# Kernel tuning notes

Hardware: AMD Instinct MI355X
Metric: run time of the kernel (lower is better)

The kernel has to match this reference:

```python
import jax, jax.numpy as jnp
import numpy as np

N_NODE = 2000
N_EDGE = 100000
N_REL2 = 102  # num_relation * 2
D_IN = 64
N_TRI = 500000


def _triangles(src, dst, N):
    """Faithful numpy port of triangle_list: for each edge (a,c) intersect
    out-neighbors of a with in-neighbors of c via sorted edge lists + searchsorted.
    Returns (edge_ab, edge_bc, edge_ac) edge-index triples."""
    E = len(src)
    src = src.astype(np.int64); dst = dst.astype(np.int64)
    in_order = np.argsort(src * N + dst, kind='stable')   # edges sorted by (a,b)
    out_order = np.argsort(dst * N + src, kind='stable')  # edges sorted by (c,b)
    deg_in = np.bincount(src, minlength=N)
    deg_out = np.bincount(dst, minlength=N)
    neighbor_out = dst[in_order]
    neighbor_in = src[out_order]
    cum_in = np.concatenate([[0], np.cumsum(deg_in)])
    cum_out = np.concatenate([[0], np.cumsum(deg_out)])
    # candidate b's: out-neighbors of a, replicated per edge (a,c)
    cnt_a = deg_in[src]
    ce = np.repeat(np.arange(E), cnt_a)
    offs = np.arange(cnt_a.sum()) - np.repeat(np.cumsum(cnt_a) - cnt_a, cnt_a)
    pos = np.repeat(cum_in[src], cnt_a) + offs
    b = neighbor_out[pos]
    ab_cand = in_order[pos]
    # boundary: in-neighbors of c, replicated per edge (globally sorted via N*segment offset)
    cnt_c = deg_out[dst]
    se = np.repeat(np.arange(E), cnt_c)
    offs2 = np.arange(cnt_c.sum()) - np.repeat(np.cumsum(cnt_c) - cnt_c, cnt_c)
    pos2 = np.repeat(cum_out[dst], cnt_c) + offs2
    boundary = neighbor_in[pos2] + N * se
    bc_order = out_order[pos2]
    key = b + N * ce
    left = np.searchsorted(boundary, key, side='left')
    right = np.searchsorted(boundary, key, side='right')
    count = right - left
    rep = np.repeat(np.arange(len(count)), count)
    within = np.arange(count.sum()) - np.repeat(np.cumsum(count) - count, count)
    return ab_cand[rep], bc_order[left[rep] + within], ce[rep]


def setup_inputs() -> dict:
    rng = np.random.default_rng(0)
    src = rng.integers(0, N_NODE, N_EDGE)
    dst = rng.integers(0, N_NODE, N_EDGE)
    edge_type = rng.integers(0, N_REL2, N_EDGE)
    ab, bc, ac = _triangles(src, dst, N_NODE)
    if len(ab) == 0:  # pathological fallback
        ab = rng.integers(0, N_EDGE, N_TRI)
        bc = rng.integers(0, N_EDGE, N_TRI)
        ac = rng.integers(0, N_EDGE, N_TRI)
    sel = rng.integers(0, len(ab), N_TRI)  # fixed-size (re)sample of triangles
    s = 0.1
    return {
        'edge_type': jnp.asarray(edge_type, jnp.int64) if jax.config.jax_enable_x64 else jnp.asarray(edge_type, jnp.int32),
        'edge_ab': jnp.asarray(ab[sel], jnp.int32),
        'edge_bc': jnp.asarray(bc[sel], jnp.int32),
        'edge_ac': jnp.asarray(ac[sel], jnp.int32),
        'fact_emb': jnp.asarray(rng.standard_normal((N_REL2, D_IN)) * s, jnp.float32),
        'W1': jnp.asarray(rng.standard_normal((D_IN, D_IN)) * s, jnp.float32),
        'b1': jnp.zeros((D_IN,), jnp.float32),
        'W2': jnp.asarray(rng.standard_normal((D_IN, D_IN)) * s, jnp.float32),
        'b2': jnp.zeros((D_IN,), jnp.float32),
        'mlp_W1': jnp.asarray(rng.standard_normal((2 * D_IN, 2 * D_IN)) * s, jnp.float32),
        'mlp_b1': jnp.zeros((2 * D_IN,), jnp.float32),
        'mlp_W2': jnp.asarray(rng.standard_normal((2 * D_IN, 1)) * s, jnp.float32),
        'mlp_b2': jnp.zeros((1,), jnp.float32),
    }


def reference(edge_type, edge_ab, edge_bc, edge_ac, fact_emb,
              W1, b1, W2, b2, mlp_W1, mlp_b1, mlp_W2, mlp_b2):
    E = edge_type.shape[0]
    x0 = fact_emb[edge_type]                      # [E, d] initial edge (fact) features
    x = x0
    for W, b in ((W1, b1), (W2, b2)):
        msg = x[edge_ab] * x[edge_bc]             # [T, d] distmult triangle messages
        agg = jax.ops.segment_sum(msg, edge_ac, num_segments=E)  # scatter-add onto ac edge
        x = jax.nn.relu(agg @ W + b)              # per-layer linear + activation
    feat = jnp.concatenate([x, x0], axis=-1)      # [E, 2d] (hidden + input, concat_hidden=False)
    h = jax.nn.relu(feat @ mlp_W1 + mlp_b1)
    return (h @ mlp_W2 + mlp_b2)[:, 0]            # [E] per-edge score
```

## Files before the change

kernel.cpp:

```cpp
#include <hip/hip_runtime.h>

#define D 64
#define FPAD 65

__device__ __forceinline__ float relu_f(float v) { return v > 0.f ? v : 0.f; }

__global__ __launch_bounds__(256) void k_prep(int* __restrict__ cnt, int En,
        const float* __restrict__ fe, const float* __restrict__ W1,
        float* __restrict__ P, int nrel,
        const float* __restrict__ mW1, const float* __restrict__ mb1,
        float* __restrict__ Q, int nZ, int nP) {
    __shared__ float Wl[64 * 64];
    __shared__ float fT[64 * FPAD];
    const int tid = threadIdx.x;
    int b = blockIdx.x;

    if (b < nZ) {
        int i = (b * 256 + tid) * 4;
        if (i + 3 < En) {
            *reinterpret_cast<int4*>(cnt + i) = make_int4(0, 0, 0, 0);
        } else {
            for (int k = i; k < En; ++k) cnt[k] = 0;
        }
        return;
    }
    b -= nZ;
    if (b < nP) {
        const int npair = nrel * nrel;
        const int p0 = b * 64;

        for (int i = tid; i < 1024; i += 256)
            reinterpret_cast<float4*>(Wl)[i] = reinterpret_cast<const float4*>(W1)[i];

        for (int i = tid; i < 1024; i += 256) {
            int r = i >> 4, q = i & 15;
            int p = p0 + r;
            float4 v = make_float4(0.f, 0.f, 0.f, 0.f);
            if (p < npair) {
                int pa = p / nrel, pb = p - pa * nrel;
                float4 va = reinterpret_cast<const float4*>(fe + (size_t)pa * D)[q];
                float4 vb = reinterpret_cast<const float4*>(fe + (size_t)pb * D)[q];
                v = make_float4(va.x * vb.x, va.y * vb.y, va.z * vb.z, va.w * vb.w);
            }
            fT[(q * 4 + 0) * FPAD + r] = v.x;
            fT[(q * 4 + 1) * FPAD + r] = v.y;
            fT[(q * 4 + 2) * FPAD + r] = v.z;
            fT[(q * 4 + 3) * FPAD + r] = v.w;
        }
        __syncthreads();

        const int j0 = (tid & 15) * 4;
        const int r0 = (tid >> 4) * 4;
        float acc[4][4];
        #pragma unroll
        for (int i = 0; i < 4; ++i)
            #pragma unroll
            for (int j = 0; j < 4; ++j) acc[i][j] = 0.f;

        #pragma unroll 8
        for (int k = 0; k < 64; ++k) {
            float4 f = *reinterpret_cast<const float4*>(&fT[k * FPAD + r0]);
            float4 w = *reinterpret_cast<const float4*>(&Wl[k * 64 + j0]);
            float fa[4] = {f.x, f.y, f.z, f.w};
            float wa[4] = {w.x, w.y, w.z, w.w};
            #pragma unroll
            for (int i = 0; i < 4; ++i)
                #pragma unroll
                for (int j = 0; j < 4; ++j) acc[i][j] += fa[i] * wa[j];
        }

        #pragma unroll
        for (int i = 0; i < 4; ++i) {
            int p = p0 + r0 + i;
            if (p < npair) {
                float4 o = make_float4(acc[i][0], acc[i][1], acc[i][2], acc[i][3]);
                *reinterpret_cast<float4*>(P + (size_t)p * D + j0) = o;
            }
        }
        return;
    }
    b -= nP;
    int t = b * 2 + (tid >> 7);
    int j = tid & 127;
    float* fl = &fT[(tid >> 7) * 64];
    if (t < nrel && j < 64) fl[j] = fe[(size_t)t * D + j];
    __syncthreads();
    if (t < nrel) {
        float s = mb1[j];
        #pragma unroll 16
        for (int k = 0; k < 64; ++k)
            s += fl[k] * mW1[(size_t)(64 + k) * 128 + j];
        Q[(size_t)t * 128 + j] = s;
    }
}


__global__ void k_hist(const int* __restrict__ ac, int* __restrict__ cnt, int T) {
    int t = blockIdx.x * blockDim.x + threadIdx.x;
    if (t < T) atomicAdd(&cnt[ac[t]], 1);
}

__global__ __launch_bounds__(256) void k_scanA(const int* __restrict__ cnt,
        int* __restrict__ localExcl, int* __restrict__ blockSums, int E) {
    __shared__ int ls[256];
    const int tid = threadIdx.x;
    int base = blockIdx.x * 1024 + tid * 4;
    int a0 = 0, a1 = 0, a2 = 0, a3 = 0;
    if (base + 3 < E) {
        int4 v = *reinterpret_cast<const int4*>(cnt + base);
        a0 = v.x; a1 = v.y; a2 = v.z; a3 = v.w;
    } else {
        if (base + 0 < E) a0 = cnt[base + 0];
        if (base + 1 < E) a1 = cnt[base + 1];
        if (base + 2 < E) a2 = cnt[base + 2];
        if (base + 3 < E) a3 = cnt[base + 3];
    }
    int tsum = a0 + a1 + a2 + a3;
    ls[tid] = tsum;
    __syncthreads();
    for (int off = 1; off < 256; off <<= 1) {
        int v = (tid >= off) ? ls[tid - off] : 0;
        __syncthreads();
        ls[tid] += v;
        __syncthreads();
    }
    int excl = ls[tid] - tsum;
    if (tid == 255) blockSums[blockIdx.x] = ls[255];
    if (base + 3 < E) {
        int4 o = make_int4(excl, excl + a0, excl + a0 + a1, excl + a0 + a1 + a2);
        *reinterpret_cast<int4*>(localExcl + base) = o;
    } else {
        int run = excl;
        if (base + 0 < E) { localExcl[base + 0] = run; run += a0; }
        if (base + 1 < E) { localExcl[base + 1] = run; run += a1; }
        if (base + 2 < E) { localExcl[base + 2] = run; run += a2; }
        if (base + 3 < E) { localExcl[base + 3] = run; }
    }
}

__global__ __launch_bounds__(256) void k_scanC(const int* __restrict__ localExcl,
        const int* __restrict__ blockSums, const int* __restrict__ cnt,
        int2* __restrict__ seg, int* __restrict__ cursor, int E, int nblk) {
    __shared__ int ls[256];
    const int tid = threadIdx.x;
    int v = (tid < nblk) ? blockSums[tid] : 0;
    ls[tid] = v;
    __syncthreads();
    for (int off = 1; off < 256; off <<= 1) {
        int w = (tid >= off) ? ls[tid - off] : 0;
        __syncthreads();
        ls[tid] += w;
        __syncthreads();
    }
    int excl = ls[tid] - v;
    __syncthreads();
    ls[tid] = excl;
    __syncthreads();
    int i = blockIdx.x * blockDim.x + tid;
    if (i < E) {
        int s = localExcl[i] + ls[i >> 10];
        seg[i] = make_int2(s, cnt[i]);
        cursor[i] = s;
    }
}

__global__ void k_permute(const int* __restrict__ ab, const int* __restrict__ bc,
                          const int* __restrict__ ac, const int* __restrict__ et,
                          int* __restrict__ cursor, int2* __restrict__ tri,
                          int* __restrict__ pid, int T, int nrel) {
    int t = blockIdx.x * blockDim.x + threadIdx.x;
    if (t >= T) return;
    int a = ab[t], b = bc[t];
    int pos = atomicAdd(&cursor[ac[t]], 1);
    tri[pos] = make_int2(a, b);
    pid[pos] = et[a] * nrel + et[b];
}

__global__ __launch_bounds__(256) void k_msg1b(const int2* __restrict__ seg,
        const int* __restrict__ pid, const float* __restrict__ P,
        const float* __restrict__ b1, float* __restrict__ xb, int E, int nquad) {
    const int tid = threadIdx.x;
    const int lane = tid & 63;
    const int sub = lane & 15;
    const int grp = lane >> 4;
    const float4* __restrict__ P4 = reinterpret_cast<const float4*>(P);
    const float4 bb = reinterpret_cast<const float4*>(b1)[sub];

    for (int quad = (blockIdx.x * blockDim.x + tid) >> 6; quad * 4 < E; quad += nquad) {
        const int e = quad * 4 + grp;
        int2 sc = make_int2(0, 0);
        if (e < E) sc = seg[e];
        const int s = sc.x, c = sc.y;
        float4 acc = make_float4(0.f, 0.f, 0.f, 0.f);
        int i = 0;
        for (; i + 3 < c; i += 4) {
            int q0 = pid[s + i + 0];
            int q1 = pid[s + i + 1];
            int q2 = pid[s + i + 2];
            int q3 = pid[s + i + 3];
            float4 v0 = P4[(size_t)q0 * 16 + sub];
            float4 v1 = P4[(size_t)q1 * 16 + sub];
            float4 v2 = P4[(size_t)q2 * 16 + sub];
            float4 v3 = P4[(size_t)q3 * 16 + sub];
            acc.x += v0.x + v1.x + v2.x + v3.x;
            acc.y += v0.y + v1.y + v2.y + v3.y;
            acc.z += v0.z + v1.z + v2.z + v3.z;
            acc.w += v0.w + v1.w + v2.w + v3.w;
        }
        for (; i < c; ++i) {
            float4 v = P4[(size_t)pid[s + i] * 16 + sub];
            acc.x += v.x; acc.y += v.y; acc.z += v.z; acc.w += v.w;
        }
        if (e < E) {
            float4 o;
            o.x = relu_f(acc.x + bb.x);
            o.y = relu_f(acc.y + bb.y);
            o.z = relu_f(acc.z + bb.z);
            o.w = relu_f(acc.w + bb.w);
            reinterpret_cast<float4*>(xb + (size_t)e * D)[sub] = o;
        }
    }
}

__global__ __launch_bounds__(256) void k_msg4(const int2* __restrict__ seg,
        const int2* __restrict__ tri, const float* __restrict__ xin,
        float* __restrict__ agg, int E, int nquad) {
    const int tid = threadIdx.x;
    const int lane = tid & 63;
    const int sub = lane & 15;
    const int grp = lane >> 4;
    const float4* __restrict__ x4 = reinterpret_cast<const float4*>(xin);

    for (int quad = (blockIdx.x * blockDim.x + tid) >> 6; quad * 4 < E; quad += nquad) {
        const int e = quad * 4 + grp;
        int2 sc = make_int2(0, 0);
        if (e < E) sc = seg[e];
        const int s = sc.x, c = sc.y;
        float4 acc = make_float4(0.f, 0.f, 0.f, 0.f);
        int i = 0;
        for (; i + 3 < c; i += 4) {
            int2 p0 = tri[s + i + 0];
            int2 p1 = tri[s + i + 1];
            int2 p2 = tri[s + i + 2];
            int2 p3 = tri[s + i + 3];
            float4 va0 = x4[(size_t)p0.x * 16 + sub];
            float4 vb0 = x4[(size_t)p0.y * 16 + sub];
            float4 va1 = x4[(size_t)p1.x * 16 + sub];
            float4 vb1 = x4[(size_t)p1.y * 16 + sub];
            float4 va2 = x4[(size_t)p2.x * 16 + sub];
            float4 vb2 = x4[(size_t)p2.y * 16 + sub];
            float4 va3 = x4[(size_t)p3.x * 16 + sub];
            float4 vb3 = x4[(size_t)p3.y * 16 + sub];
            acc.x += va0.x * vb0.x; acc.y += va0.y * vb0.y;
            acc.z += va0.z * vb0.z; acc.w += va0.w * vb0.w;
            acc.x += va1.x * vb1.x; acc.y += va1.y * vb1.y;
            acc.z += va1.z * vb1.z; acc.w += va1.w * vb1.w;
            acc.x += va2.x * vb2.x; acc.y += va2.y * vb2.y;
            acc.z += va2.z * vb2.z; acc.w += va2.w * vb2.w;
            acc.x += va3.x * vb3.x; acc.y += va3.y * vb3.y;
            acc.z += va3.z * vb3.z; acc.w += va3.w * vb3.w;
        }
        for (; i < c; ++i) {
            int2 p = tri[s + i];
            float4 va = x4[(size_t)p.x * 16 + sub];
            float4 vb = x4[(size_t)p.y * 16 + sub];
            acc.x += va.x * vb.x;
            acc.y += va.y * vb.y;
            acc.z += va.z * vb.z;
            acc.w += va.w * vb.w;
        }
        if (e < E)
            reinterpret_cast<float4*>(agg + (size_t)e * D)[sub] = acc;
    }
}

__global__ __launch_bounds__(256) void k_linmlp(const float* __restrict__ agg,
        const int* __restrict__ et, const float* __restrict__ Q,
        const float* __restrict__ W2, const float* __restrict__ b2,
        const float* __restrict__ mW1, const float* __restrict__ mW2,
        const float* __restrict__ mb2, float* __restrict__ out, int E) {
    __shared__ float Wl[64 * 64];
    __shared__ float fT[64 * FPAD];
    const int tid = threadIdx.x;
    const int row0 = blockIdx.x * 64;
    const int j0 = (tid & 15) * 4;
    const int r0 = (tid >> 4) * 4;

    for (int i = tid; i < 1024; i += 256)
        reinterpret_cast<float4*>(Wl)[i] = reinterpret_cast<const float4*>(W2)[i];
    for (int i = tid; i < 1024; i += 256) {
        int r = i >> 4, q = i & 15;
        float4 v = make_float4(0.f, 0.f, 0.f, 0.f);
        if (row0 + r < E)
            v = reinterpret_cast<const float4*>(agg + (size_t)(row0 + r) * D)[q];
        fT[(q * 4 + 0) * FPAD + r] = v.x;
        fT[(q * 4 + 1) * FPAD + r] = v.y;
        fT[(q * 4 + 2) * FPAD + r] = v.z;
        fT[(q * 4 + 3) * FPAD + r] = v.w;
    }
    __syncthreads();

    float acc[4][4];
    #pragma unroll
    for (int i = 0; i < 4; ++i)
        #pragma unroll
        for (int j = 0; j < 4; ++j) acc[i][j] = 0.f;

    #pragma unroll 8
    for (int k = 0; k < 64; ++k) {
        float4 f = *reinterpret_cast<const float4*>(&fT[k * FPAD + r0]);
        float4 w = *reinterpret_cast<const float4*>(&Wl[k * 64 + j0]);
        float fa[4] = {f.x, f.y, f.z, f.w};
        float wa[4] = {w.x, w.y, w.z, w.w};
        #pragma unroll
        for (int i = 0; i < 4; ++i)
            #pragma unroll
            for (int j = 0; j < 4; ++j) acc[i][j] += fa[i] * wa[j];
    }

    {
        float4 bv = *reinterpret_cast<const float4*>(&b2[j0]);
        float ba[4] = {bv.x, bv.y, bv.z, bv.w};
        #pragma unroll
        for (int i = 0; i < 4; ++i)
            #pragma unroll
            for (int j = 0; j < 4; ++j) acc[i][j] = relu_f(acc[i][j] + ba[j]);
    }

    __syncthreads();

    #pragma unroll
    for (int i = 0; i < 4; ++i)
        #pragma unroll
        for (int j = 0; j < 4; ++j)
            fT[(j0 + j) * FPAD + (r0 + i)] = acc[i][j];
    for (int i = tid; i < 1024; i += 256) {
        int k = i >> 4, q = i & 15;
        reinterpret_cast<float4*>(Wl)[i] =
            *reinterpret_cast<const float4*>(mW1 + (size_t)k * 128 + q * 4);
    }
    __syncthreads();

    int etc_[4];
    #pragma unroll
    for (int i = 0; i < 4; ++i) {
        int row = row0 + r0 + i;
        etc_[i] = (row < E) ? et[row] : 0;
    }

    float p[4] = {0.f, 0.f, 0.f, 0.f};

    {
        float acc2[4][4];
        #pragma unroll
        for (int i = 0; i < 4; ++i)
            #pragma unroll
            for (int j = 0; j < 4; ++j) acc2[i][j] = 0.f;
        #pragma unroll 8
        for (int k = 0; k < 64; ++k) {
            float4 f = *reinterpret_cast<const float4*>(&fT[k * FPAD + r0]);
            float4 w = *reinterpret_cast<const float4*>(&Wl[k * 64 + j0]);
            float fa[4] = {f.x, f.y, f.z, f.w};
            float wa[4] = {w.x, w.y, w.z, w.w};
            #pragma unroll
            for (int i = 0; i < 4; ++i)
                #pragma unroll
                for (int j = 0; j < 4; ++j) acc2[i][j] += fa[i] * wa[j];
        }
        float4 w2v = *reinterpret_cast<const float4*>(&mW2[j0]);
        #pragma unroll
        for (int i = 0; i < 4; ++i) {
            float4 qv = *reinterpret_cast<const float4*>(&Q[(size_t)etc_[i] * 128 + j0]);
            p[i] += relu_f(acc2[i][0] + qv.x) * w2v.x;
            p[i] += relu_f(acc2[i][1] + qv.y) * w2v.y;
            p[i] += relu_f(acc2[i][2] + qv.z) * w2v.z;
            p[i] += relu_f(acc2[i][3] + qv.w) * w2v.w;
        }
    }
    __syncthreads();
    for (int i = tid; i < 1024; i += 256) {
        int k = i >> 4, q = i & 15;
        reinterpret_cast<float4*>(Wl)[i] =
            *reinterpret_cast<const float4*>(mW1 + (size_t)k * 128 + 64 + q * 4);
    }
    __syncthreads();
    {
        float acc2[4][4];
        #pragma unroll
        for (int i = 0; i < 4; ++i)
            #pragma unroll
            for (int j = 0; j < 4; ++j) acc2[i][j] = 0.f;
        #pragma unroll 8
        for (int k = 0; k < 64; ++k) {
            float4 f = *reinterpret_cast<const float4*>(&fT[k * FPAD + r0]);
            float4 w = *reinterpret_cast<const float4*>(&Wl[k * 64 + j0]);
            float fa[4] = {f.x, f.y, f.z, f.w};
            float wa[4] = {w.x, w.y, w.z, w.w};
            #pragma unroll
            for (int i = 0; i < 4; ++i)
                #pragma unroll
                for (int j = 0; j < 4; ++j) acc2[i][j] += fa[i] * wa[j];
        }
        float4 w2v = *reinterpret_cast<const float4*>(&mW2[64 + j0]);
        #pragma unroll
        for (int i = 0; i < 4; ++i) {
            float4 qv = *reinterpret_cast<const float4*>(&Q[(size_t)etc_[i] * 128 + 64 + j0]);
            p[i] += relu_f(acc2[i][0] + qv.x) * w2v.x;
            p[i] += relu_f(acc2[i][1] + qv.y) * w2v.y;
            p[i] += relu_f(acc2[i][2] + qv.z) * w2v.z;
            p[i] += relu_f(acc2[i][3] + qv.w) * w2v.w;
        }
    }

    const float bias2 = mb2[0];
    #pragma unroll
    for (int i = 0; i < 4; ++i) {
        float s = p[i];
        s += __shfl_xor(s, 1, 64);
        s += __shfl_xor(s, 2, 64);
        s += __shfl_xor(s, 4, 64);
        s += __shfl_xor(s, 8, 64);
        if ((tid & 15) == 0) {
            int row = row0 + r0 + i;
            if (row < E) out[row] = s + bias2;
        }
    }
}

extern "C" void kernel_launch(void* const* d_in, const int* in_sizes, int n_in,
                              void* d_out, int out_size, void* d_ws, size_t ws_size,
                              hipStream_t stream) {
    const int*   edge_type = (const int*)d_in[0];
    const int*   ab        = (const int*)d_in[1];
    const int*   bc        = (const int*)d_in[2];
    const int*   ac        = (const int*)d_in[3];
    const float* fe        = (const float*)d_in[4];
    const float* W1        = (const float*)d_in[5];
    const float* b1        = (const float*)d_in[6];
    const float* W2        = (const float*)d_in[7];
    const float* b2        = (const float*)d_in[8];
    const float* mW1       = (const float*)d_in[9];
    const float* mb1       = (const float*)d_in[10];
    const float* mW2       = (const float*)d_in[11];
    const float* mb2       = (const float*)d_in[12];

    const int E = in_sizes[0];
    const int T = in_sizes[1];
    const int nrel = in_sizes[4] / D;
    const int npair = nrel * nrel;
    float* out = (float*)d_out;

    char* p = (char*)d_ws;
    float* xb   = (float*)p;   p += (size_t)E * D * sizeof(float);
    float* agg  = (float*)p;   p += (size_t)E * D * sizeof(float);
    float* P    = (float*)p;   p += (size_t)npair * D * sizeof(float);
    float* Q    = (float*)p;   p += (size_t)nrel * 128 * sizeof(float);
    int* cnt    = (int*)p;     p += (size_t)E * sizeof(int);
    int* lexcl  = (int*)p;     p += (size_t)E * sizeof(int);
    int* cursor = (int*)p;     p += (size_t)E * sizeof(int);
    int* bsums  = (int*)p;     p += 256 * sizeof(int);
    int2* seg   = (int2*)p;    p += (size_t)E * sizeof(int2);
    int2* tri   = (int2*)p;    p += (size_t)T * sizeof(int2);
    int* pid    = (int*)p;     p += (size_t)T * sizeof(int);

    const int nblkA = (E + 1023) / 1024;
    const int nZ = (E + 1023) / 1024;
    const int nP = (npair + 63) / 64;
    const int nQb = (nrel + 1) / 2;

    k_prep<<<nZ + nP + nQb, 256, 0, stream>>>(cnt, E, fe, W1, P, nrel, mW1, mb1, Q, nZ, nP);
    k_hist<<<(T + 255) / 256, 256, 0, stream>>>(ac, cnt, T);
    k_scanA<<<nblkA, 256, 0, stream>>>(cnt, lexcl, bsums, E);
    k_scanC<<<(E + 255) / 256, 256, 0, stream>>>(lexcl, bsums, cnt, seg, cursor, E, nblkA);
    k_permute<<<(T + 255) / 256, 256, 0, stream>>>(ab, bc, ac, edge_type, cursor, tri, pid, T, nrel);

    const int MSG_BLOCKS = 2048;
    const int nquad = MSG_BLOCKS * 256 / 64;
    k_msg1b<<<MSG_BLOCKS, 256, 0, stream>>>(seg, pid, P, b1, xb, E, nquad);
    k_msg4<<<MSG_BLOCKS, 256, 0, stream>>>(seg, tri, xb, agg, E, nquad);
    k_linmlp<<<(E + 63) / 64, 256, 0, stream>>>(agg, edge_type, Q, W2, b2, mW1, mW2, mb2, out, E);
}
```

Measured before the change: 164.4 us.

## Sort edges by triangle count per block for balanced wavefronts; retile MLP GEMM

k_scanC now also does a per-1024-edge-block counting sort of edges by triangle count (capped at 64), writing an order array. Both message kernels walk edges through that order, so the four edges sharing a wavefront have similar loop trip counts and less divergence. Separately, the MLP stage in k_linmlp is retiled to compute all 128 hidden columns in one pass over two K-halves with 8x4 register tiles, replacing two 64-column passes. The cost is an extra indirection load per edge, scattered output writes, and shared-memory atomics in the scan.

```diff
diff --git a/kernel.cpp b/kernel.cpp
--- a/kernel.cpp
+++ b/kernel.cpp
@@ -140,8 +140,10 @@
 
 __global__ __launch_bounds__(256) void k_scanC(const int* __restrict__ localExcl,
         const int* __restrict__ blockSums, const int* __restrict__ cnt,
-        int2* __restrict__ seg, int* __restrict__ cursor, int E, int nblk) {
+        int2* __restrict__ seg, int* __restrict__ cursor, int* __restrict__ order,
+        int E, int nblk) {
     __shared__ int ls[256];
+    __shared__ int bh[65];
     const int tid = threadIdx.x;
     int v = (tid < nblk) ? blockSums[tid] : 0;
     ls[tid] = v;
@@ -155,12 +157,48 @@
     int excl = ls[tid] - v;
     __syncthreads();
     ls[tid] = excl;
-    __syncthreads();
-    int i = blockIdx.x * blockDim.x + tid;
-    if (i < E) {
-        int s = localExcl[i] + ls[i >> 10];
-        seg[i] = make_int2(s, cnt[i]);
-        cursor[i] = s;
+    if (tid < 65) bh[tid] = 0;
+    __syncthreads();
+    const int myoff = ls[blockIdx.x];
+
+    const int base = blockIdx.x * 1024;
+    const int idx0 = base + tid * 4;
+    int c0 = 0, c1 = 0, c2 = 0, c3 = 0;
+    if (idx0 + 3 < E) {
+        int4 cv = *reinterpret_cast<const int4*>(cnt + idx0);
+        c0 = cv.x; c1 = cv.y; c2 = cv.z; c3 = cv.w;
+    } else {
+        if (idx0 + 0 < E) c0 = cnt[idx0 + 0];
+        if (idx0 + 1 < E) c1 = cnt[idx0 + 1];
+        if (idx0 + 2 < E) c2 = cnt[idx0 + 2];
+        if (idx0 + 3 < E) c3 = cnt[idx0 + 3];
+    }
+    int ca[4] = {c0, c1, c2, c3};
+    #pragma unroll
+    for (int k = 0; k < 4; ++k) {
+        int i = idx0 + k;
+        if (i < E) {
+            int s = localExcl[i] + myoff;
+            seg[i] = make_int2(s, ca[k]);
+            cursor[i] = s;
+            int bk = ca[k] < 64 ? ca[k] : 64;
+            atomicAdd(&bh[bk], 1);
+        }
+    }
+    __syncthreads();
+    if (tid == 0) {
+        int run = 0;
+        for (int k = 0; k < 65; ++k) { int t = bh[k]; bh[k] = run; run += t; }
+    }
+    __syncthreads();
+    #pragma unroll
+    for (int k = 0; k < 4; ++k) {
+        int i = idx0 + k;
+        if (i < E) {
+            int bk = ca[k] < 64 ? ca[k] : 64;
+            int pos = atomicAdd(&bh[bk], 1);
+            order[base + pos] = i;
+        }
     }
 }
 
@@ -177,8 +215,9 @@
 }
 
 __global__ __launch_bounds__(256) void k_msg1b(const int2* __restrict__ seg,
-        const int* __restrict__ pid, const float* __restrict__ P,
-        const float* __restrict__ b1, float* __restrict__ xb, int E, int nquad) {
+        const int* __restrict__ order, const int* __restrict__ pid,
+        const float* __restrict__ P, const float* __restrict__ b1,
+        float* __restrict__ xb, int E, int nquad) {
     const int tid = threadIdx.x;
     const int lane = tid & 63;
     const int sub = lane & 15;
@@ -187,9 +226,10 @@
     const float4 bb = reinterpret_cast<const float4*>(b1)[sub];
 
     for (int quad = (blockIdx.x * blockDim.x + tid) >> 6; quad * 4 < E; quad += nquad) {
-        const int e = quad * 4 + grp;
+        const int idx = quad * 4 + grp;
+        int e = -1;
         int2 sc = make_int2(0, 0);
-        if (e < E) sc = seg[e];
+        if (idx < E) { e = order[idx]; sc = seg[e]; }
         const int s = sc.x, c = sc.y;
         float4 acc = make_float4(0.f, 0.f, 0.f, 0.f);
         int i = 0;
@@ -211,7 +251,7 @@
             float4 v = P4[(size_t)pid[s + i] * 16 + sub];
             acc.x += v.x; acc.y += v.y; acc.z += v.z; acc.w += v.w;
         }
-        if (e < E) {
+        if (e >= 0) {
             float4 o;
             o.x = relu_f(acc.x + bb.x);
             o.y = relu_f(acc.y + bb.y);
@@ -223,8 +263,8 @@
 }
 
 __global__ __launch_bounds__(256) void k_msg4(const int2* __restrict__ seg,
-        const int2* __restrict__ tri, const float* __restrict__ xin,
-        float* __restrict__ agg, int E, int nquad) {
+        const int* __restrict__ order, const int2* __restrict__ tri,
+        const float* __restrict__ xin, float* __restrict__ agg, int E, int nquad) {
     const int tid = threadIdx.x;
     const int lane = tid & 63;
     const int sub = lane & 15;
@@ -232,9 +272,10 @@
     const float4* __restrict__ x4 = reinterpret_cast<const float4*>(xin);
 
     for (int quad = (blockIdx.x * blockDim.x + tid) >> 6; quad * 4 < E; quad += nquad) {
-        const int e = quad * 4 + grp;
+        const int idx = quad * 4 + grp;
+        int e = -1;
         int2 sc = make_int2(0, 0);
-        if (e < E) sc = seg[e];
+        if (idx < E) { e = order[idx]; sc = seg[e]; }
         const int s = sc.x, c = sc.y;
         float4 acc = make_float4(0.f, 0.f, 0.f, 0.f);
         int i = 0;
@@ -269,7 +310,7 @@
             acc.z += va.z * vb.z;
             acc.w += va.w * vb.w;
         }
-        if (e < E)
+        if (e >= 0)
             reinterpret_cast<float4*>(agg + (size_t)e * D)[sub] = acc;
     }
 }
@@ -279,12 +320,12 @@
         const float* __restrict__ W2, const float* __restrict__ b2,
         const float* __restrict__ mW1, const float* __restrict__ mW2,
         const float* __restrict__ mb2, float* __restrict__ out, int E) {
-    __shared__ float Wl[64 * 64];
+    __shared__ float Wl[32 * 128];
     __shared__ float fT[64 * FPAD];
     const int tid = threadIdx.x;
     const int row0 = blockIdx.x * 64;
-    const int j0 = (tid & 15) * 4;
-    const int r0 = (tid >> 4) * 4;
+    const int j0A = (tid & 15) * 4;
+    const int r0A = (tid >> 4) * 4;
 
     for (int i = tid; i < 1024; i += 256)
         reinterpret_cast<float4*>(Wl)[i] = reinterpret_cast<const float4*>(W2)[i];
@@ -308,8 +349,8 @@
 
     #pragma unroll 8
     for (int k = 0; k < 64; ++k) {
-        float4 f = *reinterpret_cast<const float4*>(&fT[k * FPAD + r0]);
-        float4 w = *reinterpret_cast<const float4*>(&Wl[k * 64 + j0]);
+        float4 f = *reinterpret_cast<const float4*>(&fT[k * FPAD + r0A]);
+        float4 w = *reinterpret_cast<const float4*>(&Wl[k * 64 + j0A]);
         float fa[4] = {f.x, f.y, f.z, f.w};
         float wa[4] = {w.x, w.y, w.z, w.w};
         #pragma unroll
@@ -319,111 +360,80 @@
     }
 
     {
-        float4 bv = *reinterpret_cast<const float4*>(&b2[j0]);
+        float4 bv = *reinterpret_cast<const float4*>(&b2[j0A]);
         float ba[4] = {bv.x, bv.y, bv.z, bv.w};
         #pragma unroll
         for (int i = 0; i < 4; ++i)
             #pragma unroll
             for (int j = 0; j < 4; ++j) acc[i][j] = relu_f(acc[i][j] + ba[j]);
     }
-
     __syncthreads();
 
     #pragma unroll
     for (int i = 0; i < 4; ++i)
         #pragma unroll
         for (int j = 0; j < 4; ++j)
-            fT[(j0 + j) * FPAD + (r0 + i)] = acc[i][j];
-    for (int i = tid; i < 1024; i += 256) {
-        int k = i >> 4, q = i & 15;
+            fT[(j0A + j) * FPAD + (r0A + i)] = acc[i][j];
+    for (int i = tid; i < 1024; i += 256)
+        reinterpret_cast<float4*>(Wl)[i] = reinterpret_cast<const float4*>(mW1)[i];
+    __syncthreads();
+
+    const int j0 = (tid & 31) * 4;
+    const int r0 = (tid >> 5) * 8;
+    float acc2[8][4];
+    #pragma unroll
+    for (int i = 0; i < 8; ++i)
+        #pragma unroll
+        for (int j = 0; j < 4; ++j) acc2[i][j] = 0.f;
+
+    #pragma unroll 4
+    for (int k = 0; k < 32; ++k) {
+        float4 fA = *reinterpret_cast<const float4*>(&fT[k * FPAD + r0]);
+        float4 fB = *reinterpret_cast<const float4*>(&fT[k * FPAD + r0 + 4]);
+        float4 w = *reinterpret_cast<const float4*>(&Wl[k * 128 + j0]);
+        float fa[8] = {fA.x, fA.y, fA.z, fA.w, fB.x, fB.y, fB.z, fB.w};
+        float wa[4] = {w.x, w.y, w.z, w.w};
+        #pragma unroll
+        for (int i = 0; i < 8; ++i)
+            #pragma unroll
+            for (int j = 0; j < 4; ++j) acc2[i][j] += fa[i] * wa[j];
+    }
+    __syncthreads();
+    for (int i = tid; i < 1024; i += 256)
         reinterpret_cast<float4*>(Wl)[i] =
-            *reinterpret_cast<const float4*>(mW1 + (size_t)k * 128 + q * 4);
-    }
-    __syncthreads();
-
-    int etc_[4];
-    #pragma unroll
-    for (int i = 0; i < 4; ++i) {
+            reinterpret_cast<const float4*>(mW1 + 32 * 128)[i];
+    __syncthreads();
+    #pragma unroll 4
+    for (int k = 0; k < 32; ++k) {
+        float4 fA = *reinterpret_cast<const float4*>(&fT[(32 + k) * FPAD + r0]);
+        float4 fB = *reinterpret_cast<const float4*>(&fT[(32 + k) * FPAD + r0 + 4]);
+        float4 w = *reinterpret_cast<const float4*>(&Wl[k * 128 + j0]);
+        float fa[8] = {fA.x, fA.y, fA.z, fA.w, fB.x, fB.y, fB.z, fB.w};
+        float wa[4] = {w.x, w.y, w.z, w.w};
+        #pragma unroll
+        for (int i = 0; i < 8; ++i)
+            #pragma unroll
+            for (int j = 0; j < 4; ++j) acc2[i][j] += fa[i] * wa[j];
+    }
+
+    float4 w2v = *reinterpret_cast<const float4*>(&mW2[j0]);
+    const float bias2 = mb2[0];
+    #pragma unroll
+    for (int i = 0; i < 8; ++i) {
         int row = row0 + r0 + i;
-        etc_[i] = (row < E) ? et[row] : 0;
-    }
-
-    float p[4] = {0.f, 0.f, 0.f, 0.f};
-
-    {
-        float acc2[4][4];
-        #pragma unroll
-        for (int i = 0; i < 4; ++i)
-            #pragma unroll
-            for (int j = 0; j < 4; ++j) acc2[i][j] = 0.f;
-        #pragma unroll 8
-        for (int k = 0; k < 64; ++k) {
-            float4 f = *reinterpret_cast<const float4*>(&fT[k * FPAD + r0]);
-            float4 w = *reinterpret_cast<const float4*>(&Wl[k * 64 + j0]);
-            float fa[4] = {f.x, f.y, f.z, f.w};
-            float wa[4] = {w.x, w.y, w.z, w.w};
-            #pragma unroll
-            for (int i = 0; i < 4; ++i)
-                #pragma unroll
-                for (int j = 0; j < 4; ++j) acc2[i][j] += fa[i] * wa[j];
-        }
-        float4 w2v = *reinterpret_cast<const float4*>(&mW2[j0]);
-        #pragma unroll
-        for (int i = 0; i < 4; ++i) {
-            float4 qv = *reinterpret_cast<const float4*>(&Q[(size_t)etc_[i] * 128 + j0]);
-            p[i] += relu_f(acc2[i][0] + qv.x) * w2v.x;
-            p[i] += relu_f(acc2[i][1] + qv.y) * w2v.y;
-            p[i] += relu_f(acc2[i][2] + qv.z) * w2v.z;
-            p[i] += relu_f(acc2[i][3] + qv.w) * w2v.w;
-        }
-    }
-    __syncthreads();
-    for (int i = tid; i < 1024; i += 256) {
-        int k = i >> 4, q = i & 15;
-        reinterpret_cast<float4*>(Wl)[i] =
-            *reinterpret_cast<const float4*>(mW1 + (size_t)k * 128 + 64 + q * 4);
-    }
-    __syncthreads();
-    {
-        float acc2[4][4];
-        #pragma unroll
-        for (int i = 0; i < 4; ++i)
-            #pragma unroll
-            for (int j = 0; j < 4; ++j) acc2[i][j] = 0.f;
-        #pragma unroll 8
-        for (int k = 0; k < 64; ++k) {
-            float4 f = *reinterpret_cast<const float4*>(&fT[k * FPAD + r0]);
-            float4 w = *reinterpret_cast<const float4*>(&Wl[k * 64 + j0]);
-            float fa[4] = {f.x, f.y, f.z, f.w};
-            float wa[4] = {w.x, w.y, w.z, w.w};
-            #pragma unroll
-            for (int i = 0; i < 4; ++i)
-                #pragma unroll
-                for (int j = 0; j < 4; ++j) acc2[i][j] += fa[i] * wa[j];
-        }
-        float4 w2v = *reinterpret_cast<const float4*>(&mW2[64 + j0]);
-        #pragma unroll
-        for (int i = 0; i < 4; ++i) {
-            float4 qv = *reinterpret_cast<const float4*>(&Q[(size_t)etc_[i] * 128 + 64 + j0]);
-            p[i] += relu_f(acc2[i][0] + qv.x) * w2v.x;
-            p[i] += relu_f(acc2[i][1] + qv.y) * w2v.y;
-            p[i] += relu_f(acc2[i][2] + qv.z) * w2v.z;
-            p[i] += relu_f(acc2[i][3] + qv.w) * w2v.w;
-        }
-    }
-
-    const float bias2 = mb2[0];
-    #pragma unroll
-    for (int i = 0; i < 4; ++i) {
-        float s = p[i];
-        s += __shfl_xor(s, 1, 64);
-        s += __shfl_xor(s, 2, 64);
-        s += __shfl_xor(s, 4, 64);
-        s += __shfl_xor(s, 8, 64);
-        if ((tid & 15) == 0) {
-            int row = row0 + r0 + i;
-            if (row < E) out[row] = s + bias2;
-        }
+        int ete = (row < E) ? et[row] : 0;
+        float4 qv = *reinterpret_cast<const float4*>(&Q[(size_t)ete * 128 + j0]);
+        float h0 = relu_f(acc2[i][0] + qv.x);
+        float h1 = relu_f(acc2[i][1] + qv.y);
+        float h2 = relu_f(acc2[i][2] + qv.z);
+        float h3 = relu_f(acc2[i][3] + qv.w);
+        float p = h0 * w2v.x + h1 * w2v.y + h2 * w2v.z + h3 * w2v.w;
+        p += __shfl_xor(p, 1, 64);
+        p += __shfl_xor(p, 2, 64);
+        p += __shfl_xor(p, 4, 64);
+        p += __shfl_xor(p, 8, 64);
+        p += __shfl_xor(p, 16, 64);
+        if ((tid & 31) == 0 && row < E) out[row] = p + bias2;
     }
 }
 
@@ -458,6 +468,7 @@
     int* cnt    = (int*)p;     p += (size_t)E * sizeof(int);
     int* lexcl  = (int*)p;     p += (size_t)E * sizeof(int);
     int* cursor = (int*)p;     p += (size_t)E * sizeof(int);
+    int* order  = (int*)p;     p += (size_t)E * sizeof(int);
     int* bsums  = (int*)p;     p += 256 * sizeof(int);
     int2* seg   = (int2*)p;    p += (size_t)E * sizeof(int2);
     int2* tri   = (int2*)p;    p += (size_t)T * sizeof(int2);
@@ -471,12 +482,12 @@
     k_prep<<<nZ + nP + nQb, 256, 0, stream>>>(cnt, E, fe, W1, P, nrel, mW1, mb1, Q, nZ, nP);
     k_hist<<<(T + 255) / 256, 256, 0, stream>>>(ac, cnt, T);
     k_scanA<<<nblkA, 256, 0, stream>>>(cnt, lexcl, bsums, E);
-    k_scanC<<<(E + 255) / 256, 256, 0, stream>>>(lexcl, bsums, cnt, seg, cursor, E, nblkA);
+    k_scanC<<<nblkA, 256, 0, stream>>>(lexcl, bsums, cnt, seg, cursor, order, E, nblkA);
     k_permute<<<(T + 255) / 256, 256, 0, stream>>>(ab, bc, ac, edge_type, cursor, tri, pid, T, nrel);
 
     const int MSG_BLOCKS = 2048;
     const int nquad = MSG_BLOCKS * 256 / 64;
-    k_msg1b<<<MSG_BLOCKS, 256, 0, stream>>>(seg, pid, P, b1, xb, E, nquad);
-    k_msg4<<<MSG_BLOCKS, 256, 0, stream>>>(seg, tri, xb, agg, E, nquad);
+    k_msg1b<<<MSG_BLOCKS, 256, 0, stream>>>(seg, order, pid, P, b1, xb, E, nquad);
+    k_msg4<<<MSG_BLOCKS, 256, 0, stream>>>(seg, order, tri, xb, agg, E, nquad);
     k_linmlp<<<(E + 63) / 64, 256, 0, stream>>>(agg, edge_type, Q, W2, b2, mW1, mW2, mb2, out, E);
 }
```

Measured after the change: 192.5 us. 1.17x slower.
